# Kernel optimization log

Hardware: AMD Instinct MI355X
Metric: run time of the kernel (lower is better)

The kernel has to match this reference:

```python
import jax, jax.numpy as jnp
import numpy as np

B, N, F_IN = 8, 4096, 32
NRP = 1024
D_MODEL = 512
K = 64  # max_num_neighbors
STAGE_CFG = ((1024, 0.05), (256, 0.3), (64, 0.5))  # (num_samples=ceil(0.25*N_in), radius)


def fps(pos, m):
    """Farthest point sampling of m points from pos (N,3), deterministic start at 0."""
    d = jnp.sum((pos - pos[0]) ** 2, axis=-1)
    idxs = jnp.zeros((m,), jnp.int32)
    def body(i, carry):
        idxs, d = carry
        nxt = jnp.argmax(d).astype(jnp.int32)
        d = jnp.minimum(d, jnp.sum((pos - pos[nxt]) ** 2, axis=-1))
        return (idxs.at[i].set(nxt), d)
    idxs, _ = jax.lax.fori_loop(1, m, body, (idxs, d))
    return idxs


def apply_mlp(h, ws, bs):
    for w, b in zip(ws[:-1], bs[:-1]):
        h = jax.nn.relu(h @ w + b)
    return h @ ws[-1] + bs[-1]


def sa_stage(x, pos, m, r, ws, bs):
    """SAModule: FPS -> radius neighbors (<=K) -> PointNetConv (gather, MLP, max-scatter)."""
    idx = jax.vmap(lambda p: fps(p, m))(pos)                          # (B,m)
    pos_s = jnp.take_along_axis(pos, idx[..., None], axis=1)          # (B,m,3)
    d2 = jnp.sum((pos_s[:, :, None, :] - pos[:, None, :, :]) ** 2, -1)  # (B,m,N)
    neg = jnp.where(d2 <= r * r, -d2, -jnp.inf)
    vals, nbr = jax.lax.top_k(neg, K)                                 # (B,m,K) nearest within r
    valid = vals > -jnp.inf                                           # self always valid (d2=0)
    x_j = jax.vmap(lambda xb, nb: xb[nb])(x, nbr)                     # (B,m,K,F) gather
    p_j = jax.vmap(lambda pb, nb: pb[nb])(pos, nbr)                   # (B,m,K,3)
    h = jnp.concatenate([x_j, p_j - pos_s[:, :, None, :]], axis=-1)   # message input
    h = apply_mlp(h, ws, bs)
    h = jnp.where(valid[..., None], h, -jnp.inf)
    return jnp.max(h, axis=2), pos_s                                  # max aggregation


def _forward(point_cloud_features, point_cloud, emb_table, point_id_emb, stage_params):
    x = emb_table[point_cloud_features[..., 0]]                       # (B,N,F_IN)
    x = x.at[:, :NRP].add(point_id_emb)
    pos = point_cloud
    for (m, r), (ws, bs) in zip(STAGE_CFG, stage_params):
        x, pos = sa_stage(x, pos, m, r, ws, bs)
    return x, pos                                                     # (B,64,D_MODEL), (B,64,3)


def setup_inputs() -> dict:
    key = jax.random.key(0)
    ks = iter(jax.random.split(key, 64))
    def nrm(shape, s=0.05):
        return s * jax.random.normal(next(ks), shape, dtype=jnp.float32)
    inp = {
        "point_cloud_features": jax.random.randint(next(ks), (B, N, 1), 0, 3),
        "point_cloud": jax.random.uniform(next(ks), (B, N, 3), dtype=jnp.float32),
        "emb_table": nrm((3, F_IN), 1.0),
        "point_id_emb": nrm((1, NRP, F_IN), 1.0),
    }
    dims = {"s1": [3 + F_IN, 64, 64, 64], "s2": [64 + 3, 128, 128, 256], "s3": [256 + 3, 256, 512, D_MODEL]}
    for s, d in dims.items():
        for i in range(3):
            inp[f"{s}w{i}"] = nrm((d[i], d[i + 1]))
            inp[f"{s}b{i}"] = jnp.zeros((d[i + 1],), jnp.float32)
    return inp


def reference(point_cloud_features, point_cloud, emb_table, point_id_emb,
              s1w0, s1b0, s1w1, s1b1, s1w2, s1b2,
              s2w0, s2b0, s2w1, s2b1, s2w2, s2b2,
              s3w0, s3b0, s3w1, s3b1, s3w2, s3b2):
    stage_params = [
        ([s1w0, s1w1, s1w2], [s1b0, s1b1, s1b2]),
        ([s2w0, s2w1, s2w2], [s2b0, s2b1, s2b2]),
        ([s3w0, s3w1, s3w2], [s3b0, s3b1, s3b2]),
    ]
    return _forward(point_cloud_features, point_cloud, emb_table, point_id_emb, stage_params)
```

## Files before the change

### kernel.cpp

```cpp
#include <hip/hip_runtime.h>

#define DEVI static __device__ __forceinline__

constexpr int B = 8;
constexpr int N0 = 4096;
constexpr int KNB = 64;

typedef float f32x2 __attribute__((ext_vector_type(2)));
typedef float f32x4 __attribute__((ext_vector_type(4)));
typedef short bf16x8 __attribute__((ext_vector_type(8)));

DEVI float dist2f(float ax, float ay, float az, float bx, float by, float bz) {
#pragma clang fp contract(off)
  float dx = ax - bx;
  float dy = ay - by;
  float dz = az - bz;
  return (dx * dx + dy * dy) + dz * dz;
}
DEVI f32x2 dist2v(f32x2 ax, f32x2 ay, f32x2 az, float bx, float by, float bz) {
#pragma clang fp contract(off)
  f32x2 dx = ax - bx;
  f32x2 dy = ay - by;
  f32x2 dz = az - bz;
  return (dx * dx + dy * dy) + dz * dz;
}

DEVI unsigned long long packMinKey(float v, int i) {
  return ((unsigned long long)__float_as_uint(v) << 32) | (unsigned int)i;
}

template <int CTRL, int RM>
DEVI float dppMaxF32(float v) {
  int o = __builtin_amdgcn_update_dpp(__float_as_int(v), __float_as_int(v),
                                      CTRL, RM, 0xf, false);
  return fmaxf(v, __int_as_float(o));
}
DEVI float waveMaxF32(float v) {
  v = dppMaxF32<0x111, 0xf>(v);
  v = dppMaxF32<0x112, 0xf>(v);
  v = dppMaxF32<0x114, 0xf>(v);
  v = dppMaxF32<0x118, 0xf>(v);
  v = dppMaxF32<0x142, 0xa>(v);
  v = dppMaxF32<0x143, 0xc>(v);
  return __int_as_float(__builtin_amdgcn_readlane(__float_as_int(v), 63));
}
template <int CTRL, int RM>
DEVI unsigned dppMinU32(unsigned v) {
  int o = __builtin_amdgcn_update_dpp((int)v, (int)v, CTRL, RM, 0xf, false);
  unsigned ov = (unsigned)o;
  return v < ov ? v : ov;
}
DEVI unsigned waveMinU32(unsigned v) {
  v = dppMinU32<0x111, 0xf>(v);
  v = dppMinU32<0x112, 0xf>(v);
  v = dppMinU32<0x114, 0xf>(v);
  v = dppMinU32<0x118, 0xf>(v);
  v = dppMinU32<0x142, 0xa>(v);
  v = dppMinU32<0x143, 0xc>(v);
  return (unsigned)__builtin_amdgcn_readlane((int)v, 63);
}

DEVI unsigned short bfhi(float x) {
  unsigned u = __float_as_uint(x);
  return (unsigned short)((u + 0x7FFFu + ((u >> 16) & 1u)) >> 16);
}
DEVI float bf2f(unsigned short h) { return __uint_as_float(((unsigned)h) << 16); }
DEVI void mkfrag(const float* p, bf16x8& hi, bf16x8& lo) {
#pragma unroll
  for (int e = 0; e < 8; ++e) {
    float x = p[e];
    unsigned short h = bfhi(x);
    float r = x - bf2f(h);
    unsigned short l2 = bfhi(r);
    hi[e] = (short)h;
    lo[e] = (short)l2;
  }
}


DEVI void x0_body(const int* __restrict__ feat, const float* __restrict__ emb,
                  const float* __restrict__ pid, float* __restrict__ x0buf,
                  int bx, int t) {
  int gid = bx * 256 + t;
  if (gid >= B * N0 * 32) return;
  int c = gid & 31;
  int bn = gid >> 5;
  int n = bn & (N0 - 1);
  int f = feat[bn];
  float v = emb[f * 32 + c];
  if (n < 1024) v += pid[n * 32 + c];
  x0buf[gid] = v;
}

template <int NPTS, int M, int BLK>
DEVI void fps_body(char* smem, const float* __restrict__ pos,
                   float* __restrict__ pos_out, int b, int t) {
  constexpr int EPT = NPTS / BLK;
  constexpr int EP2 = EPT / 2;
  constexpr int NW = BLK / 64;
  float4* posl = (float4*)smem;
  float4* outp = (float4*)(smem + (size_t)NPTS * 16);
  unsigned long long* redk =
      (unsigned long long*)(smem + (size_t)(NPTS + M) * 16);
  const float* pb = pos + (size_t)b * NPTS * 3;
  f32x2 px[EP2], py[EP2], pz[EP2], d[EP2];
#pragma unroll
  for (int e = 0; e < EP2; ++e) {
    int i0 = t + (2 * e) * BLK;
    int i1 = t + (2 * e + 1) * BLK;
    float x0 = pb[i0 * 3 + 0], y0 = pb[i0 * 3 + 1], z0 = pb[i0 * 3 + 2];
    float x1 = pb[i1 * 3 + 0], y1 = pb[i1 * 3 + 1], z1 = pb[i1 * 3 + 2];
    px[e] = (f32x2){x0, x1};
    py[e] = (f32x2){y0, y1};
    pz[e] = (f32x2){z0, z1};
    posl[i0] = make_float4(x0, y0, z0, 0.f);
    posl[i1] = make_float4(x1, y1, z1, 0.f);
  }
  float sx = pb[0], sy = pb[1], sz = pb[2];
  if (t == 0) outp[0] = make_float4(sx, sy, sz, 0.f);
  f32x2 m2 = (f32x2){-1.f, -1.f};
#pragma unroll
  for (int e = 0; e < EP2; ++e) {
    d[e] = dist2v(px[e], py[e], pz[e], sx, sy, sz);
    m2.x = fmaxf(m2.x, d[e].x);
    m2.y = fmaxf(m2.y, d[e].y);
  }
  for (int it = 1; it < M; ++it) {
    const float vstar = waveMaxF32(fmaxf(m2.x, m2.y));
    unsigned cand = 0xffffffffu;
#pragma unroll
    for (int e = 0; e < EP2; ++e) {
      unsigned c0 = (d[e].x == vstar) ? (unsigned)(t + (2 * e) * BLK) : 0xffffffffu;
      unsigned c1 = (d[e].y == vstar) ? (unsigned)(t + (2 * e + 1) * BLK) : 0xffffffffu;
      cand = cand < c0 ? cand : c0;
      cand = cand < c1 ? cand : c1;
    }
    cand = waveMinU32(cand);
    unsigned sel;
    if constexpr (NW > 1) {
      if ((t & 63) == 0) {
        unsigned long long key =
            ((unsigned long long)__float_as_uint(vstar) << 32) |
            (unsigned)(0x7fffffffu - cand);
        redk[(it & 1) * NW + (t >> 6)] = key;
      }
      __syncthreads();
      unsigned long long kk = redk[(it & 1) * NW + 0];
#pragma unroll
      for (int w = 1; w < NW; ++w) {
        unsigned long long o = redk[(it & 1) * NW + w];
        kk = (kk > o) ? kk : o;
      }
      sel = 0x7fffffffu - (unsigned)(kk & 0xffffffffULL);
    } else {
      sel = cand;
    }
    float4 sp = posl[sel];
    if (t == 0) outp[it] = sp;
    m2 = (f32x2){-1.f, -1.f};
#pragma unroll
    for (int e = 0; e < EP2; ++e) {
      f32x2 nd = dist2v(px[e], py[e], pz[e], sp.x, sp.y, sp.z);
      d[e].x = fminf(d[e].x, nd.x);
      d[e].y = fminf(d[e].y, nd.y);
      m2.x = fmaxf(m2.x, d[e].x);
      m2.y = fmaxf(m2.y, d[e].y);
    }
  }
  if constexpr (NW > 1) __syncthreads();
  for (int m = t; m < M; m += BLK) {
    float4 q = outp[m];
    pos_out[(size_t)(b * M + m) * 3 + 0] = q.x;
    pos_out[(size_t)(b * M + m) * 3 + 1] = q.y;
    pos_out[(size_t)(b * M + m) * 3 + 2] = q.z;
  }
}

template <int NPTS, int M>
DEVI void radius_body(char* smem, const float* __restrict__ pos,
                      const float* __restrict__ pos_s, float r2,
                      int* __restrict__ nbr, int* __restrict__ cnt, int blk,
                      int t) {
  unsigned long long* candkey = (unsigned long long*)smem;
  int* ctrp = (int*)(smem + (size_t)NPTS * 8);
  const int b = blk / M;
  const float* pb = pos + (size_t)b * NPTS * 3;
  const float cx = pos_s[(size_t)blk * 3 + 0];
  const float cy = pos_s[(size_t)blk * 3 + 1];
  const float cz = pos_s[(size_t)blk * 3 + 2];
  if (t == 0) *ctrp = 0;
  __syncthreads();
  for (int j = t; j < NPTS; j += 256) {
    float d2 = dist2f(pb[j * 3 + 0], pb[j * 3 + 1], pb[j * 3 + 2], cx, cy, cz);
    if (d2 <= r2) {
      int p = atomicAdd(ctrp, 1);
      candkey[p] = packMinKey(d2, j);
      if (p < KNB) nbr[(size_t)blk * KNB + p] = j;
    }
  }
  __syncthreads();
  const int c = *ctrp;
  if (c <= KNB) {
    if (t == 0) cnt[blk] = c;
    return;
  }
  for (int s = t; s < c; s += 256) {
    unsigned long long mykey = candkey[s];
    int rank = 0;
#pragma unroll 4
    for (int j = 0; j < c; ++j) {
      rank += (candkey[j] < mykey) ? 1 : 0;
    }
    if (rank < KNB)
      nbr[(size_t)blk * KNB + rank] = (int)(unsigned)(mykey & 0xffffffffULL);
  }
  if (t == 0) cnt[blk] = KNB;
}

DEVI void conv1_body(char* smem, const float* __restrict__ x0buf,
                     const float* __restrict__ pos,
                     const float* __restrict__ pos_s,
                     const int* __restrict__ nbr, const int* __restrict__ cntp,
                     const float* __restrict__ w0, const float* __restrict__ b0,
                     const float* __restrict__ w1, const float* __restrict__ b1,
                     const float* __restrict__ w2, const float* __restrict__ b2,
                     float* __restrict__ x1, int blk, int t) {
  float(*ins)[36] = (float(*)[36])smem;
  float(*hh)[65] = (float(*)[65])(smem + 576);
  float(*sred)[65] = (float(*)[65])(smem + 1616);
  const int slot = t >> 6;
  const int ch = t & 63;
  const int b = blk >> 10;
  const int c = cntp[blk];
  const float cx = pos_s[(size_t)blk * 3 + 0];
  const float cy = pos_s[(size_t)blk * 3 + 1];
  const float cz = pos_s[(size_t)blk * 3 + 2];
  float best = -__builtin_inff();
  for (int r0 = 0; r0 < c; r0 += 4) {
    const int r = r0 + slot;
    const bool act = r < c;
    const int j = nbr[(size_t)blk * KNB + (act ? r : 0)];
    if (ch < 32) {
      ins[slot][ch] = x0buf[((size_t)(b * N0) + j) * 32 + ch];
    } else if (ch < 35) {
      float pv = pos[((size_t)(b * N0) + j) * 3 + (ch - 32)];
      float cv = (ch == 32) ? cx : (ch == 33) ? cy : cz;
      ins[slot][ch] = pv - cv;
    }
    __syncthreads();
    float v = b0[ch];
#pragma unroll
    for (int i = 0; i < 35; ++i) v = fmaf(ins[slot][i], w0[i * 64 + ch], v);
    v = fmaxf(v, 0.f);
    hh[slot][ch] = v;
    __syncthreads();
    float v2 = b1[ch];
#pragma unroll
    for (int i = 0; i < 64; ++i) v2 = fmaf(hh[slot][i], w1[i * 64 + ch], v2);
    v2 = fmaxf(v2, 0.f);
    __syncthreads();
    hh[slot][ch] = v2;
    __syncthreads();
    float v3 = b2[ch];
#pragma unroll
    for (int i = 0; i < 64; ++i) v3 = fmaf(hh[slot][i], w2[i * 64 + ch], v3);
    if (act) best = fmaxf(best, v3);
    __syncthreads();
  }
  sred[slot][ch] = best;
  __syncthreads();
  if (t < 64) {
    float v = sred[0][t];
#pragma unroll
    for (int s = 1; s < 4; ++s) v = fmaxf(v, sred[s][t]);
    x1[(size_t)blk * 64 + t] = v;
  }
}

DEVI void conv2_mfma_body(char* smem, const float* __restrict__ x1,
                          const float* __restrict__ pos1,
                          const float* __restrict__ pos2,
                          const int* __restrict__ nbr,
                          const int* __restrict__ cntp,
                          const unsigned short* __restrict__ w0h,
                          const float* __restrict__ b0,
                          const unsigned short* __restrict__ w1h,
                          const float* __restrict__ b1,
                          const unsigned short* __restrict__ w2h,
                          const float* __restrict__ b2,
                          float* __restrict__ x2, int blk, int t) {
  float(*h1)[132] = (float(*)[132])smem;
  float(*h2)[132] = (float(*)[132])(smem + 33792);
  float* red = (float*)smem;
  const int b = blk >> 8;
  const int c = cntp[blk];
  const int w = t >> 6;
  const int lane = t & 63;
  const int cb = lane & 15;
  const int kb = lane >> 4;
  const int mrow = w * 16 + cb;
  const int jrow = nbr[(size_t)blk * KNB + (mrow < c ? mrow : c - 1)];
  const float* xrow = x1 + ((size_t)(b * 1024) + jrow) * 64;
  const float cx = pos2[(size_t)blk * 3 + 0];
  const float cy = pos2[(size_t)blk * 3 + 1];
  const float cz = pos2[(size_t)blk * 3 + 2];

  f32x4 acc1[8];
#pragma unroll
  for (int nt = 0; nt < 8; ++nt) acc1[nt] = (f32x4){0.f, 0.f, 0.f, 0.f};
#pragma unroll
  for (int ks = 0; ks < 2; ++ks) {
    float xv[8];
    *(float4*)&xv[0] = *(const float4*)&xrow[ks * 32 + kb * 8];
    *(float4*)&xv[4] = *(const float4*)&xrow[ks * 32 + kb * 8 + 4];
    bf16x8 ahi, alo;
    mkfrag(xv, ahi, alo);
#pragma unroll
    for (int nt = 0; nt < 8; ++nt) {
      size_t off = ((size_t)(nt * 3 + ks) * 64 + lane) * 8;
      bf16x8 bhi = *(const bf16x8*)(w0h + off);
      acc1[nt] = __builtin_amdgcn_mfma_f32_16x16x32_bf16(ahi, bhi, acc1[nt], 0, 0, 0);
      acc1[nt] = __builtin_amdgcn_mfma_f32_16x16x32_bf16(alo, bhi, acc1[nt], 0, 0, 0);
    }
  }
  {
    float xv[8] = {0.f, 0.f, 0.f, 0.f, 0.f, 0.f, 0.f, 0.f};
    if (kb == 0) {
      xv[0] = pos1[((size_t)(b * 1024) + jrow) * 3 + 0] - cx;
      xv[1] = pos1[((size_t)(b * 1024) + jrow) * 3 + 1] - cy;
      xv[2] = pos1[((size_t)(b * 1024) + jrow) * 3 + 2] - cz;
    }
    bf16x8 ahi, alo;
    mkfrag(xv, ahi, alo);
#pragma unroll
    for (int nt = 0; nt < 8; ++nt) {
      size_t off = ((size_t)(nt * 3 + 2) * 64 + lane) * 8;
      bf16x8 bhi = *(const bf16x8*)(w0h + off);
      acc1[nt] = __builtin_amdgcn_mfma_f32_16x16x32_bf16(ahi, bhi, acc1[nt], 0, 0, 0);
      acc1[nt] = __builtin_amdgcn_mfma_f32_16x16x32_bf16(alo, bhi, acc1[nt], 0, 0, 0);
    }
  }
  {
    const int mw = w * 16 + kb * 4;
#pragma unroll
    for (int nt = 0; nt < 8; ++nt) {
      float bias = b0[nt * 16 + cb];
#pragma unroll
      for (int r = 0; r < 4; ++r)
        h1[mw + r][nt * 16 + cb] = fmaxf(acc1[nt][r] + bias, 0.f);
    }
  }

  f32x4 acc2[8];
#pragma unroll
  for (int nt = 0; nt < 8; ++nt) acc2[nt] = (f32x4){0.f, 0.f, 0.f, 0.f};
#pragma unroll
  for (int ks = 0; ks < 4; ++ks) {
    bf16x8 ahi, alo;
    mkfrag(&h1[mrow][ks * 32 + kb * 8], ahi, alo);
#pragma unroll
    for (int nt = 0; nt < 8; ++nt) {
      size_t off = ((size_t)(nt * 4 + ks) * 64 + lane) * 8;
      bf16x8 bhi = *(const bf16x8*)(w1h + off);
      acc2[nt] = __builtin_amdgcn_mfma_f32_16x16x32_bf16(ahi, bhi, acc2[nt], 0, 0, 0);
      acc2[nt] = __builtin_amdgcn_mfma_f32_16x16x32_bf16(alo, bhi, acc2[nt], 0, 0, 0);
    }
  }
  {
    const int mw = w * 16 + kb * 4;
#pragma unroll
    for (int nt = 0; nt < 8; ++nt) {
      float bias = b1[nt * 16 + cb];
#pragma unroll
      for (int r = 0; r < 4; ++r)
        h2[mw + r][nt * 16 + cb] = fmaxf(acc2[nt][r] + bias, 0.f);
    }
  }

  f32x4 acc3[16];
#pragma unroll
  for (int nt = 0; nt < 16; ++nt) acc3[nt] = (f32x4){0.f, 0.f, 0.f, 0.f};
#pragma unroll
  for (int ks = 0; ks < 4; ++ks) {
    bf16x8 ahi, alo;
    mkfrag(&h2[mrow][ks * 32 + kb * 8], ahi, alo);
#pragma unroll
    for (int nt = 0; nt < 16; ++nt) {
      size_t off = ((size_t)(nt * 4 + ks) * 64 + lane) * 8;
      bf16x8 bhi = *(const bf16x8*)(w2h + off);
      acc3[nt] = __builtin_amdgcn_mfma_f32_16x16x32_bf16(ahi, bhi, acc3[nt], 0, 0, 0);
      acc3[nt] = __builtin_amdgcn_mfma_f32_16x16x32_bf16(alo, bhi, acc3[nt], 0, 0, 0);
    }
  }
  __syncthreads();
  {
    const int mw = w * 16 + kb * 4;
#pragma unroll
    for (int nt = 0; nt < 16; ++nt) {
      float bias = b2[nt * 16 + cb];
      float mx = -__builtin_inff();
#pragma unroll
      for (int r = 0; r < 4; ++r) {
        if (mw + r < c) mx = fmaxf(mx, acc3[nt][r] + bias);
      }
      red[(w * 4 + kb) * 256 + nt * 16 + cb] = mx;
    }
  }
  __syncthreads();
  {
    float v = red[t];
#pragma unroll
    for (int g = 1; g < 16; ++g) v = fmaxf(v, red[g * 256 + t]);
    x2[(size_t)blk * 256 + t] = v;
  }
}


__global__ void __launch_bounds__(256) l1_kernel(
    const float* __restrict__ pos, float* __restrict__ pos1,
    const int* __restrict__ feat, const float* __restrict__ emb,
    const float* __restrict__ pid, float* __restrict__ x0buf) {
  __shared__ __attribute__((aligned(16))) char smem[81984];
  if (blockIdx.x < 8) {
    fps_body<4096, 1024, 256>(smem, pos, pos1, blockIdx.x, threadIdx.x);
  } else {
    x0_body(feat, emb, pid, x0buf, blockIdx.x - 8, threadIdx.x);
  }
}

__global__ void __launch_bounds__(256) l2_kernel(
    const float* __restrict__ pos1, float* __restrict__ pos2,
    const float* __restrict__ pos, float r2a, int* __restrict__ nbr1,
    int* __restrict__ cnt1) {
  __shared__ __attribute__((aligned(16))) char smem[33024];
  if (blockIdx.x < 8) {
    fps_body<1024, 256, 256>(smem, pos1, pos2, blockIdx.x, threadIdx.x);
  } else {
    radius_body<4096, 1024>(smem, pos, pos1, r2a, nbr1, cnt1, blockIdx.x - 8,
                            threadIdx.x);
  }
}

__global__ void __launch_bounds__(256) l3_kernel(
    const float* __restrict__ pos2, float* __restrict__ pos3, float r2b,
    int* __restrict__ nbr2, int* __restrict__ cnt2,
    const float* __restrict__ pos1, const float* __restrict__ x0buf,
    const float* __restrict__ pos, const int* __restrict__ nbr1,
    const int* __restrict__ cnt1, const float* __restrict__ w0,
    const float* __restrict__ b0, const float* __restrict__ w1,
    const float* __restrict__ b1, const float* __restrict__ w2,
    const float* __restrict__ b2, float* __restrict__ x1) {
  __shared__ __attribute__((aligned(16))) char smem[8448];
  if (blockIdx.x < 8) {
    if (threadIdx.x < 64)
      fps_body<256, 64, 64>(smem, pos2, pos3, blockIdx.x, threadIdx.x);
  } else if (blockIdx.x < 8 + 2048) {
    radius_body<1024, 256>(smem, pos1, pos2, r2b, nbr2, cnt2, blockIdx.x - 8,
                           threadIdx.x);
  } else {
    conv1_body(smem, x0buf, pos, pos1, nbr1, cnt1, w0, b0, w1, b1, w2, b2, x1,
               blockIdx.x - (8 + 2048), threadIdx.x);
  }
}

__global__ void __launch_bounds__(256) l4_kernel(
    const float* __restrict__ pos2, const float* __restrict__ pos3, float r2c,
    int* __restrict__ nbr3, int* __restrict__ cnt3,
    const float* __restrict__ x1, const float* __restrict__ pos1,
    const int* __restrict__ nbr2, const int* __restrict__ cnt2,
    const unsigned short* __restrict__ v0h, const float* __restrict__ b0,
    const unsigned short* __restrict__ v1h, const float* __restrict__ b1,
    const unsigned short* __restrict__ v2h, const float* __restrict__ b2,
    float* __restrict__ x2) {
  __shared__ __attribute__((aligned(16))) char smem[67584];
  if (blockIdx.x < 512) {
    radius_body<256, 64>(smem, pos2, pos3, r2c, nbr3, cnt3, blockIdx.x,
                         threadIdx.x);
  } else {
    conv2_mfma_body(smem, x1, pos1, pos2, nbr2, cnt2, v0h, b0, v1h, b1, v2h,
                    b2, x2, blockIdx.x - 512, threadIdx.x);
  }
}

__global__ void __launch_bounds__(256) pack_kernel(
    const float* __restrict__ W, int Kreal, int KS, int N,
    unsigned short* __restrict__ hi, unsigned short* __restrict__ lo) {
  int gid = blockIdx.x * 256 + threadIdx.x;
  int total = (N / 16) * KS * 64 * 8;
  if (gid >= total) return;
  int e = gid & 7;
  int l = (gid >> 3) & 63;
  int rest = gid >> 9;
  int ks = rest % KS;
  int nt = rest / KS;
  int n = nt * 16 + (l & 15);
  int k = ks * 32 + (l >> 4) * 8 + e;
  float val = (k < Kreal) ? W[(size_t)k * N + n] : 0.f;
  unsigned short h = bfhi(val);
  float r = val - bf2f(h);
  hi[gid] = h;
  lo[gid] = bfhi(r);
}

__global__ void __launch_bounds__(256) conv3_mfma(
    const float* __restrict__ x2, const float* __restrict__ pos2,
    const float* __restrict__ pos3, const int* __restrict__ nbr,
    const int* __restrict__ cntp,
    const unsigned short* __restrict__ w0h, const float* __restrict__ b0,
    const unsigned short* __restrict__ w1h, const float* __restrict__ b1,
    const unsigned short* __restrict__ w2h, const float* __restrict__ b2,
    float* __restrict__ out) {
  __shared__ __attribute__((aligned(16))) float h1s[64 * 268];
  __shared__ __attribute__((aligned(16))) float h2cs[64 * 140];
  const int blk = blockIdx.x;
  const int t = threadIdx.x;
  const int b = blk >> 6;
  const int c = cntp[blk];
  const int w = t >> 6;
  const int lane = t & 63;
  const int cb = lane & 15;
  const int kb = lane >> 4;
  const float cx = pos3[(size_t)blk * 3 + 0];
  const float cy = pos3[(size_t)blk * 3 + 1];
  const float cz = pos3[(size_t)blk * 3 + 2];
  const int mrow = w * 16 + cb;
  const int jrow = nbr[(size_t)blk * KNB + (mrow < c ? mrow : c - 1)];
  const float* xrow = x2 + ((size_t)(b * 256) + jrow) * 256;

  f32x4 acc1[16];
#pragma unroll
  for (int nt = 0; nt < 16; ++nt) acc1[nt] = (f32x4){0.f, 0.f, 0.f, 0.f};
#pragma unroll
  for (int ks = 0; ks < 8; ++ks) {
    float xv[8];
    *(float4*)&xv[0] = *(const float4*)&xrow[ks * 32 + kb * 8];
    *(float4*)&xv[4] = *(const float4*)&xrow[ks * 32 + kb * 8 + 4];
    bf16x8 ahi, alo;
    mkfrag(xv, ahi, alo);
#pragma unroll
    for (int nt = 0; nt < 16; ++nt) {
      size_t off = ((size_t)(nt * 9 + ks) * 64 + lane) * 8;
      bf16x8 bhi = *(const bf16x8*)(w0h + off);
      acc1[nt] = __builtin_amdgcn_mfma_f32_16x16x32_bf16(ahi, bhi, acc1[nt], 0, 0, 0);
      acc1[nt] = __builtin_amdgcn_mfma_f32_16x16x32_bf16(alo, bhi, acc1[nt], 0, 0, 0);
    }
  }
  {
    float xv[8] = {0.f, 0.f, 0.f, 0.f, 0.f, 0.f, 0.f, 0.f};
    if (kb == 0) {
      xv[0] = pos2[((size_t)(b * 256) + jrow) * 3 + 0] - cx;
      xv[1] = pos2[((size_t)(b * 256) + jrow) * 3 + 1] - cy;
      xv[2] = pos2[((size_t)(b * 256) + jrow) * 3 + 2] - cz;
    }
    bf16x8 ahi, alo;
    mkfrag(xv, ahi, alo);
#pragma unroll
    for (int nt = 0; nt < 16; ++nt) {
      size_t off = ((size_t)(nt * 9 + 8) * 64 + lane) * 8;
      bf16x8 bhi = *(const bf16x8*)(w0h + off);
      acc1[nt] = __builtin_amdgcn_mfma_f32_16x16x32_bf16(ahi, bhi, acc1[nt], 0, 0, 0);
      acc1[nt] = __builtin_amdgcn_mfma_f32_16x16x32_bf16(alo, bhi, acc1[nt], 0, 0, 0);
    }
  }
  {
    const int mw = w * 16 + kb * 4;
#pragma unroll
    for (int nt = 0; nt < 16; ++nt) {
      float bias = b0[nt * 16 + cb];
#pragma unroll
      for (int r = 0; r < 4; ++r)
        h1s[(mw + r) * 268 + nt * 16 + cb] = fmaxf(acc1[nt][r] + bias, 0.f);
    }
  }

  f32x4 acc3[32];
#pragma unroll
  for (int nt = 0; nt < 32; ++nt) acc3[nt] = (f32x4){0.f, 0.f, 0.f, 0.f};
  for (int ch = 0; ch < 4; ++ch) {
    f32x4 acc2[8];
#pragma unroll
    for (int nt = 0; nt < 8; ++nt) acc2[nt] = (f32x4){0.f, 0.f, 0.f, 0.f};
#pragma unroll
    for (int ks = 0; ks < 8; ++ks) {
      bf16x8 ahi, alo;
      mkfrag(&h1s[mrow * 268 + ks * 32 + kb * 8], ahi, alo);
#pragma unroll
      for (int nt = 0; nt < 8; ++nt) {
        size_t off = ((size_t)((ch * 8 + nt) * 8 + ks) * 64 + lane) * 8;
        bf16x8 bhi = *(const bf16x8*)(w1h + off);
        acc2[nt] = __builtin_amdgcn_mfma_f32_16x16x32_bf16(ahi, bhi, acc2[nt], 0, 0, 0);
        acc2[nt] = __builtin_amdgcn_mfma_f32_16x16x32_bf16(alo, bhi, acc2[nt], 0, 0, 0);
      }
    }
    {
      const int mw = w * 16 + kb * 4;
#pragma unroll
      for (int nt = 0; nt < 8; ++nt) {
        float bias = b1[ch * 128 + nt * 16 + cb];
#pragma unroll
        for (int r = 0; r < 4; ++r)
          h2cs[(mw + r) * 140 + nt * 16 + cb] = fmaxf(acc2[nt][r] + bias, 0.f);
      }
    }
#pragma unroll
    for (int ks3 = 0; ks3 < 4; ++ks3) {
      bf16x8 ahi, alo;
      mkfrag(&h2cs[mrow * 140 + ks3 * 32 + kb * 8], ahi, alo);
#pragma unroll
      for (int nt = 0; nt < 32; ++nt) {
        size_t off = ((size_t)(nt * 16 + ch * 4 + ks3) * 64 + lane) * 8;
        bf16x8 bhi = *(const bf16x8*)(w2h + off);
        acc3[nt] = __builtin_amdgcn_mfma_f32_16x16x32_bf16(ahi, bhi, acc3[nt], 0, 0, 0);
        acc3[nt] = __builtin_amdgcn_mfma_f32_16x16x32_bf16(alo, bhi, acc3[nt], 0, 0, 0);
      }
    }
  }

  __syncthreads();
  float* redw = h1s;
  {
    const int mw = w * 16 + kb * 4;
#pragma unroll
    for (int nt = 0; nt < 32; ++nt) {
      float bias = b2[nt * 16 + cb];
      float mx = -__builtin_inff();
#pragma unroll
      for (int r = 0; r < 4; ++r) {
        if (mw + r < c) mx = fmaxf(mx, acc3[nt][r] + bias);
      }
      redw[(w * 4 + kb) * 512 + nt * 16 + cb] = mx;
    }
  }
  __syncthreads();
#pragma unroll
  for (int half = 0; half < 2; ++half) {
    int col = t + half * 256;
    float v = redw[col];
#pragma unroll
    for (int g = 1; g < 16; ++g) v = fmaxf(v, redw[g * 512 + col]);
    out[(size_t)blk * 512 + col] = v;
  }
}

extern "C" void kernel_launch(void* const* d_in, const int* in_sizes, int n_in,
                              void* d_out, int out_size, void* d_ws, size_t ws_size,
                              hipStream_t stream) {
  const int* feat = (const int*)d_in[0];
  const float* pos = (const float*)d_in[1];
  const float* emb = (const float*)d_in[2];
  const float* pid = (const float*)d_in[3];
  const float* s1w0 = (const float*)d_in[4];
  const float* s1b0 = (const float*)d_in[5];
  const float* s1w1 = (const float*)d_in[6];
  const float* s1b1 = (const float*)d_in[7];
  const float* s1w2 = (const float*)d_in[8];
  const float* s1b2 = (const float*)d_in[9];
  const float* s2w0 = (const float*)d_in[10];
  const float* s2b0 = (const float*)d_in[11];
  const float* s2w1 = (const float*)d_in[12];
  const float* s2b1 = (const float*)d_in[13];
  const float* s2w2 = (const float*)d_in[14];
  const float* s2b2 = (const float*)d_in[15];
  const float* s3w0 = (const float*)d_in[16];
  const float* s3b0 = (const float*)d_in[17];
  const float* s3w1 = (const float*)d_in[18];
  const float* s3b1 = (const float*)d_in[19];
  const float* s3w2 = (const float*)d_in[20];
  const float* s3b2 = (const float*)d_in[21];
  (void)in_sizes; (void)n_in; (void)out_size; (void)ws_size;

  char* ws = (char*)d_ws;
  size_t off = 0;
  auto alloc = [&](size_t nbytes) {
    void* p = ws + off;
    off = (off + nbytes + 255) & ~(size_t)255;
    return p;
  };
  float* x0 = (float*)alloc((size_t)B * N0 * 32 * 4);
  float* pos1 = (float*)alloc((size_t)B * 1024 * 3 * 4);
  int* nbr1 = (int*)alloc((size_t)B * 1024 * KNB * 4);
  int* cnt1 = (int*)alloc((size_t)B * 1024 * 4);
  float* x1 = (float*)alloc((size_t)B * 1024 * 64 * 4);
  float* pos2 = (float*)alloc((size_t)B * 256 * 3 * 4);
  int* nbr2 = (int*)alloc((size_t)B * 256 * KNB * 4);
  int* cnt2 = (int*)alloc((size_t)B * 256 * 4);
  float* x2 = (float*)alloc((size_t)B * 256 * 256 * 4);
  int* nbr3 = (int*)alloc((size_t)B * 64 * KNB * 4);
  int* cnt3 = (int*)alloc((size_t)B * 64 * 4);
  const int T0 = 16 * 9 * 64 * 8;
  const int T1 = 32 * 8 * 64 * 8;
  const int T2 = 32 * 16 * 64 * 8;
  unsigned short* w0h = (unsigned short*)alloc((size_t)T0 * 2);
  unsigned short* w0l = (unsigned short*)alloc((size_t)T0 * 2);
  unsigned short* w1h = (unsigned short*)alloc((size_t)T1 * 2);
  unsigned short* w1l = (unsigned short*)alloc((size_t)T1 * 2);
  unsigned short* w2h = (unsigned short*)alloc((size_t)T2 * 2);
  unsigned short* w2l = (unsigned short*)alloc((size_t)T2 * 2);
  const int U0 = 8 * 3 * 64 * 8;
  const int U1 = 8 * 4 * 64 * 8;
  const int U2 = 16 * 4 * 64 * 8;
  unsigned short* v0h = (unsigned short*)alloc((size_t)U0 * 2);
  unsigned short* v0l = (unsigned short*)alloc((size_t)U0 * 2);
  unsigned short* v1h = (unsigned short*)alloc((size_t)U1 * 2);
  unsigned short* v1l = (unsigned short*)alloc((size_t)U1 * 2);
  unsigned short* v2h = (unsigned short*)alloc((size_t)U2 * 2);
  unsigned short* v2l = (unsigned short*)alloc((size_t)U2 * 2);

  float* xout = (float*)d_out;
  float* pos3 = xout + (size_t)B * 64 * 512;

  const float r2a = (float)(0.05 * 0.05);
  const float r2b = (float)(0.3 * 0.3);
  const float r2c = (float)(0.5 * 0.5);

  pack_kernel<<<(T0 + 255) / 256, 256, 0, stream>>>(s3w0, 259, 9, 256, w0h, w0l);
  pack_kernel<<<(T1 + 255) / 256, 256, 0, stream>>>(s3w1, 256, 8, 512, w1h, w1l);
  pack_kernel<<<(T2 + 255) / 256, 256, 0, stream>>>(s3w2, 512, 16, 512, w2h, w2l);
  pack_kernel<<<(U0 + 255) / 256, 256, 0, stream>>>(s2w0, 67, 3, 128, v0h, v0l);
  pack_kernel<<<(U1 + 255) / 256, 256, 0, stream>>>(s2w1, 128, 4, 128, v1h, v1l);
  pack_kernel<<<(U2 + 255) / 256, 256, 0, stream>>>(s2w2, 128, 4, 256, v2h, v2l);

  l1_kernel<<<8 + 4096, 256, 0, stream>>>(pos, pos1, feat, emb, pid, x0);
  l2_kernel<<<8 + 8192, 256, 0, stream>>>(pos1, pos2, pos, r2a, nbr1, cnt1);
  l3_kernel<<<8 + 2048 + 8192, 256, 0, stream>>>(
      pos2, pos3, r2b, nbr2, cnt2, pos1, x0, pos, nbr1, cnt1,
      s1w0, s1b0, s1w1, s1b1, s1w2, s1b2, x1);
  l4_kernel<<<512 + 2048, 256, 0, stream>>>(
      pos2, pos3, r2c, nbr3, cnt3, x1, pos1, nbr2, cnt2,
      v0h, s2b0, v1h, s2b1, v2h, s2b2, x2);
  conv3_mfma<<<B * 64, 256, 0, stream>>>(x2, pos2, pos3, nbr3, cnt3,
                                         w0h, s3b0, w1h, s3b1, w2h, s3b2, xout);
}
```

Baseline: 1.280 ms.

## Fuse FPS argmax into one 64-bit wave reduction, merge weight packing into l1

The farthest-point-sampling loop now packs each lane's local max distance and its first-index candidate into a 64-bit key and runs a single wave max reduction. This replaces the separate float max reduction, equality scan and unsigned min reduction on the serial critical path. The second FPS stage now runs on a single wave of 64 threads, which removes the per-iteration __syncthreads and shared-memory merge but gives each lane four times as many points. The six weight-packing launches are folded into extra blocks of l1_kernel to cut launch overhead.

After: 1.248 ms, median of 2. 2.5% less time.

```diff
diff --git a/kernel.cpp b/kernel.cpp
--- a/kernel.cpp
+++ b/kernel.cpp
@@ -30,34 +30,23 @@
 }
 
 template <int CTRL, int RM>
-DEVI float dppMaxF32(float v) {
-  int o = __builtin_amdgcn_update_dpp(__float_as_int(v), __float_as_int(v),
-                                      CTRL, RM, 0xf, false);
-  return fmaxf(v, __int_as_float(o));
-}
-DEVI float waveMaxF32(float v) {
-  v = dppMaxF32<0x111, 0xf>(v);
-  v = dppMaxF32<0x112, 0xf>(v);
-  v = dppMaxF32<0x114, 0xf>(v);
-  v = dppMaxF32<0x118, 0xf>(v);
-  v = dppMaxF32<0x142, 0xa>(v);
-  v = dppMaxF32<0x143, 0xc>(v);
-  return __int_as_float(__builtin_amdgcn_readlane(__float_as_int(v), 63));
-}
-template <int CTRL, int RM>
-DEVI unsigned dppMinU32(unsigned v) {
-  int o = __builtin_amdgcn_update_dpp((int)v, (int)v, CTRL, RM, 0xf, false);
-  unsigned ov = (unsigned)o;
-  return v < ov ? v : ov;
-}
-DEVI unsigned waveMinU32(unsigned v) {
-  v = dppMinU32<0x111, 0xf>(v);
-  v = dppMinU32<0x112, 0xf>(v);
-  v = dppMinU32<0x114, 0xf>(v);
-  v = dppMinU32<0x118, 0xf>(v);
-  v = dppMinU32<0x142, 0xa>(v);
-  v = dppMinU32<0x143, 0xc>(v);
-  return (unsigned)__builtin_amdgcn_readlane((int)v, 63);
+DEVI unsigned long long dppMaxU64(unsigned long long k) {
+  unsigned lo = (unsigned)k, hi = (unsigned)(k >> 32);
+  unsigned mlo = (unsigned)__builtin_amdgcn_update_dpp((int)lo, (int)lo, CTRL, RM, 0xf, false);
+  unsigned mhi = (unsigned)__builtin_amdgcn_update_dpp((int)hi, (int)hi, CTRL, RM, 0xf, false);
+  unsigned long long o = ((unsigned long long)mhi << 32) | mlo;
+  return (k > o) ? k : o;
+}
+DEVI unsigned long long waveReduceMaxU64(unsigned long long k) {
+  k = dppMaxU64<0x111, 0xf>(k);
+  k = dppMaxU64<0x112, 0xf>(k);
+  k = dppMaxU64<0x114, 0xf>(k);
+  k = dppMaxU64<0x118, 0xf>(k);
+  k = dppMaxU64<0x142, 0xa>(k);
+  k = dppMaxU64<0x143, 0xc>(k);
+  unsigned lo = (unsigned)__builtin_amdgcn_readlane((int)(unsigned)k, 63);
+  unsigned hi = (unsigned)__builtin_amdgcn_readlane((int)(unsigned)(k >> 32), 63);
+  return ((unsigned long long)hi << 32) | lo;
 }
 
 DEVI unsigned short bfhi(float x) {
@@ -92,6 +81,23 @@
   x0buf[gid] = v;
 }
 
+DEVI void pack_body(int gid, const float* __restrict__ W, int Kreal, int KS,
+                    int N, unsigned short* __restrict__ hi,
+                    unsigned short* __restrict__ lo) {
+  int e = gid & 7;
+  int l = (gid >> 3) & 63;
+  int rest = gid >> 9;
+  int ks = rest % KS;
+  int nt = rest / KS;
+  int n = nt * 16 + (l & 15);
+  int k = ks * 32 + (l >> 4) * 8 + e;
+  float val = (k < Kreal) ? W[(size_t)k * N + n] : 0.f;
+  unsigned short h = bfhi(val);
+  float r = val - bf2f(h);
+  hi[gid] = h;
+  lo[gid] = bfhi(r);
+}
+
 template <int NPTS, int M, int BLK>
 DEVI void fps_body(char* smem, const float* __restrict__ pos,
                    float* __restrict__ pos_out, int b, int t) {
@@ -126,24 +132,22 @@
     m2.y = fmaxf(m2.y, d[e].y);
   }
   for (int it = 1; it < M; ++it) {
-    const float vstar = waveMaxF32(fmaxf(m2.x, m2.y));
+    const float lm = fmaxf(m2.x, m2.y);
     unsigned cand = 0xffffffffu;
 #pragma unroll
     for (int e = 0; e < EP2; ++e) {
-      unsigned c0 = (d[e].x == vstar) ? (unsigned)(t + (2 * e) * BLK) : 0xffffffffu;
-      unsigned c1 = (d[e].y == vstar) ? (unsigned)(t + (2 * e + 1) * BLK) : 0xffffffffu;
-      cand = cand < c0 ? cand : c0;
-      cand = cand < c1 ? cand : c1;
-    }
-    cand = waveMinU32(cand);
+      unsigned c0 = (d[e].x == lm) ? (unsigned)(t + (2 * e) * BLK) : 0xffffffffu;
+      unsigned c1 = (d[e].y == lm) ? (unsigned)(t + (2 * e + 1) * BLK) : 0xffffffffu;
+      unsigned cc = c0 < c1 ? c0 : c1;
+      cand = cand < cc ? cand : cc;
+    }
+    unsigned long long k =
+        ((unsigned long long)__float_as_uint(lm) << 32) |
+        (unsigned)(0x7fffffffu - cand);
+    k = waveReduceMaxU64(k);
     unsigned sel;
     if constexpr (NW > 1) {
-      if ((t & 63) == 0) {
-        unsigned long long key =
-            ((unsigned long long)__float_as_uint(vstar) << 32) |
-            (unsigned)(0x7fffffffu - cand);
-        redk[(it & 1) * NW + (t >> 6)] = key;
-      }
+      if ((t & 63) == 0) redk[(it & 1) * NW + (t >> 6)] = k;
       __syncthreads();
       unsigned long long kk = redk[(it & 1) * NW + 0];
 #pragma unroll
@@ -153,19 +157,20 @@
       }
       sel = 0x7fffffffu - (unsigned)(kk & 0xffffffffULL);
     } else {
-      sel = cand;
+      sel = 0x7fffffffu - (unsigned)(k & 0xffffffffULL);
     }
     float4 sp = posl[sel];
     if (t == 0) outp[it] = sp;
-    m2 = (f32x2){-1.f, -1.f};
+    f32x2 mm = (f32x2){-1.f, -1.f};
 #pragma unroll
     for (int e = 0; e < EP2; ++e) {
       f32x2 nd = dist2v(px[e], py[e], pz[e], sp.x, sp.y, sp.z);
       d[e].x = fminf(d[e].x, nd.x);
       d[e].y = fminf(d[e].y, nd.y);
-      m2.x = fmaxf(m2.x, d[e].x);
-      m2.y = fmaxf(m2.y, d[e].y);
-    }
+      mm.x = fmaxf(mm.x, d[e].x);
+      mm.y = fmaxf(mm.y, d[e].y);
+    }
+    m2 = mm;
   }
   if constexpr (NW > 1) __syncthreads();
   for (int m = t; m < M; m += BLK) {
@@ -416,16 +421,52 @@
 }
 
 
+constexpr int PK_T0 = 16 * 9 * 64 * 8;
+constexpr int PK_T1 = 32 * 8 * 64 * 8;
+constexpr int PK_T2 = 32 * 16 * 64 * 8;
+constexpr int PK_U0 = 8 * 3 * 64 * 8;
+constexpr int PK_U1 = 8 * 4 * 64 * 8;
+constexpr int PK_U2 = 16 * 4 * 64 * 8;
+constexpr int PK_TOTAL = PK_T0 + PK_T1 + PK_T2 + PK_U0 + PK_U1 + PK_U2;
+constexpr int PK_BLOCKS = PK_TOTAL / 256;
+
 __global__ void __launch_bounds__(256) l1_kernel(
     const float* __restrict__ pos, float* __restrict__ pos1,
     const int* __restrict__ feat, const float* __restrict__ emb,
-    const float* __restrict__ pid, float* __restrict__ x0buf) {
+    const float* __restrict__ pid, float* __restrict__ x0buf,
+    const float* __restrict__ s3w0, const float* __restrict__ s3w1,
+    const float* __restrict__ s3w2, const float* __restrict__ s2w0,
+    const float* __restrict__ s2w1, const float* __restrict__ s2w2,
+    unsigned short* __restrict__ w0h, unsigned short* __restrict__ w0l,
+    unsigned short* __restrict__ w1h, unsigned short* __restrict__ w1l,
+    unsigned short* __restrict__ w2h, unsigned short* __restrict__ w2l,
+    unsigned short* __restrict__ v0h, unsigned short* __restrict__ v0l,
+    unsigned short* __restrict__ v1h, unsigned short* __restrict__ v1l,
+    unsigned short* __restrict__ v2h, unsigned short* __restrict__ v2l) {
   __shared__ __attribute__((aligned(16))) char smem[81984];
-  if (blockIdx.x < 8) {
-    fps_body<4096, 1024, 256>(smem, pos, pos1, blockIdx.x, threadIdx.x);
-  } else {
-    x0_body(feat, emb, pid, x0buf, blockIdx.x - 8, threadIdx.x);
-  }
+  int bx = blockIdx.x;
+  if (bx < 8) {
+    fps_body<4096, 1024, 256>(smem, pos, pos1, bx, threadIdx.x);
+    return;
+  }
+  bx -= 8;
+  if (bx < 4096) {
+    x0_body(feat, emb, pid, x0buf, bx, threadIdx.x);
+    return;
+  }
+  bx -= 4096;
+  int gid = bx * 256 + threadIdx.x;
+  if (gid < PK_T0) { pack_body(gid, s3w0, 259, 9, 256, w0h, w0l); return; }
+  gid -= PK_T0;
+  if (gid < PK_T1) { pack_body(gid, s3w1, 256, 8, 512, w1h, w1l); return; }
+  gid -= PK_T1;
+  if (gid < PK_T2) { pack_body(gid, s3w2, 512, 16, 512, w2h, w2l); return; }
+  gid -= PK_T2;
+  if (gid < PK_U0) { pack_body(gid, s2w0, 67, 3, 128, v0h, v0l); return; }
+  gid -= PK_U0;
+  if (gid < PK_U1) { pack_body(gid, s2w1, 128, 4, 128, v1h, v1l); return; }
+  gid -= PK_U1;
+  if (gid < PK_U2) { pack_body(gid, s2w2, 128, 4, 256, v2h, v2l); return; }
 }
 
 __global__ void __launch_bounds__(256) l2_kernel(
@@ -434,7 +475,8 @@
     int* __restrict__ cnt1) {
   __shared__ __attribute__((aligned(16))) char smem[33024];
   if (blockIdx.x < 8) {
-    fps_body<1024, 256, 256>(smem, pos1, pos2, blockIdx.x, threadIdx.x);
+    if (threadIdx.x < 64)
+      fps_body<1024, 256, 64>(smem, pos1, pos2, blockIdx.x, threadIdx.x);
   } else {
     radius_body<4096, 1024>(smem, pos, pos1, r2a, nbr1, cnt1, blockIdx.x - 8,
                             threadIdx.x);
@@ -480,26 +522,6 @@
     conv2_mfma_body(smem, x1, pos1, pos2, nbr2, cnt2, v0h, b0, v1h, b1, v2h,
                     b2, x2, blockIdx.x - 512, threadIdx.x);
   }
-}
-
-__global__ void __launch_bounds__(256) pack_kernel(
-    const float* __restrict__ W, int Kreal, int KS, int N,
-    unsigned short* __restrict__ hi, unsigned short* __restrict__ lo) {
-  int gid = blockIdx.x * 256 + threadIdx.x;
-  int total = (N / 16) * KS * 64 * 8;
-  if (gid >= total) return;
-  int e = gid & 7;
-  int l = (gid >> 3) & 63;
-  int rest = gid >> 9;
-  int ks = rest % KS;
-  int nt = rest / KS;
-  int n = nt * 16 + (l & 15);
-  int k = ks * 32 + (l >> 4) * 8 + e;
-  float val = (k < Kreal) ? W[(size_t)k * N + n] : 0.f;
-  unsigned short h = bfhi(val);
-  float r = val - bf2f(h);
-  hi[gid] = h;
-  lo[gid] = bfhi(r);
 }
 
 __global__ void __launch_bounds__(256) conv3_mfma(
@@ -687,24 +709,18 @@
   float* x2 = (float*)alloc((size_t)B * 256 * 256 * 4);
   int* nbr3 = (int*)alloc((size_t)B * 64 * KNB * 4);
   int* cnt3 = (int*)alloc((size_t)B * 64 * 4);
-  const int T0 = 16 * 9 * 64 * 8;
-  const int T1 = 32 * 8 * 64 * 8;
-  const int T2 = 32 * 16 * 64 * 8;
-  unsigned short* w0h = (unsigned short*)alloc((size_t)T0 * 2);
-  unsigned short* w0l = (unsigned short*)alloc((size_t)T0 * 2);
-  unsigned short* w1h = (unsigned short*)alloc((size_t)T1 * 2);
-  unsigned short* w1l = (unsigned short*)alloc((size_t)T1 * 2);
-  unsigned short* w2h = (unsigned short*)alloc((size_t)T2 * 2);
-  unsigned short* w2l = (unsigned short*)alloc((size_t)T2 * 2);
-  const int U0 = 8 * 3 * 64 * 8;
-  const int U1 = 8 * 4 * 64 * 8;
-  const int U2 = 16 * 4 * 64 * 8;
-  unsigned short* v0h = (unsigned short*)alloc((size_t)U0 * 2);
-  unsigned short* v0l = (unsigned short*)alloc((size_t)U0 * 2);
-  unsigned short* v1h = (unsigned short*)alloc((size_t)U1 * 2);
-  unsigned short* v1l = (unsigned short*)alloc((size_t)U1 * 2);
-  unsigned short* v2h = (unsigned short*)alloc((size_t)U2 * 2);
-  unsigned short* v2l = (unsigned short*)alloc((size_t)U2 * 2);
+  unsigned short* w0h = (unsigned short*)alloc((size_t)PK_T0 * 2);
+  unsigned short* w0l = (unsigned short*)alloc((size_t)PK_T0 * 2);
+  unsigned short* w1h = (unsigned short*)alloc((size_t)PK_T1 * 2);
+  unsigned short* w1l = (unsigned short*)alloc((size_t)PK_T1 * 2);
+  unsigned short* w2h = (unsigned short*)alloc((size_t)PK_T2 * 2);
+  unsigned short* w2l = (unsigned short*)alloc((size_t)PK_T2 * 2);
+  unsigned short* v0h = (unsigned short*)alloc((size_t)PK_U0 * 2);
+  unsigned short* v0l = (unsigned short*)alloc((size_t)PK_U0 * 2);
+  unsigned short* v1h = (unsigned short*)alloc((size_t)PK_U1 * 2);
+  unsigned short* v1l = (unsigned short*)alloc((size_t)PK_U1 * 2);
+  unsigned short* v2h = (unsigned short*)alloc((size_t)PK_U2 * 2);
+  unsigned short* v2l = (unsigned short*)alloc((size_t)PK_U2 * 2);
 
   float* xout = (float*)d_out;
   float* pos3 = xout + (size_t)B * 64 * 512;
@@ -713,14 +729,9 @@
   const float r2b = (float)(0.3 * 0.3);
   const float r2c = (float)(0.5 * 0.5);
 
-  pack_kernel<<<(T0 + 255) / 256, 256, 0, stream>>>(s3w0, 259, 9, 256, w0h, w0l);
-  pack_kernel<<<(T1 + 255) / 256, 256, 0, stream>>>(s3w1, 256, 8, 512, w1h, w1l);
-  pack_kernel<<<(T2 + 255) / 256, 256, 0, stream>>>(s3w2, 512, 16, 512, w2h, w2l);
-  pack_kernel<<<(U0 + 255) / 256, 256, 0, stream>>>(s2w0, 67, 3, 128, v0h, v0l);
-  pack_kernel<<<(U1 + 255) / 256, 256, 0, stream>>>(s2w1, 128, 4, 128, v1h, v1l);
-  pack_kernel<<<(U2 + 255) / 256, 256, 0, stream>>>(s2w2, 128, 4, 256, v2h, v2l);
-
-  l1_kernel<<<8 + 4096, 256, 0, stream>>>(pos, pos1, feat, emb, pid, x0);
+  l1_kernel<<<8 + 4096 + PK_BLOCKS, 256, 0, stream>>>(
+      pos, pos1, feat, emb, pid, x0, s3w0, s3w1, s3w2, s2w0, s2w1, s2w2,
+      w0h, w0l, w1h, w1l, w2h, w2l, v0h, v0l, v1h, v1l, v2h, v2l);
   l2_kernel<<<8 + 8192, 256, 0, stream>>>(pos1, pos2, pos, r2a, nbr1, cnt1);
   l3_kernel<<<8 + 2048 + 8192, 256, 0, stream>>>(
       pos2, pos3, r2b, nbr2, cnt2, pos1, x0, pos, nbr1, cnt1,
```
